# Kernel optimization log

Measured on AMD Instinct MI355X. Metric: run time of the kernel, lower is better.

The kernel has to match this reference:

```python
import jax, jax.numpy as jnp
import numpy as np

N = 768        # particles
C0 = 16        # input L0 channels
TDIM = 8       # time embedding channels
NB = 32        # sinusoidal rbf bases
H = 32         # hidden channels per L
NITERS = 2     # diffusion iterations (hk.scan length)
RCUT = 6.0     # rbf length scale
EPS = 1e-8

_lc = np.zeros((3, 3, 3), dtype=np.float32)
_lc[0, 1, 2] = _lc[1, 2, 0] = _lc[2, 0, 1] = 1.0
_lc[0, 2, 1] = _lc[2, 1, 0] = _lc[1, 0, 2] = -1.0
LEVI_CIVITA = jnp.asarray(_lc)


def setup_inputs() -> dict:
    key = jax.random.key(0)
    ks = jax.random.split(key, 20)
    s = 0.05
    inp = {
        "positions":   jax.random.normal(ks[0], (N, 3)),
        "features_L0": jax.random.normal(ks[1], (N, C0, 1)),
        "tw1": s * jax.random.normal(ks[2], (1, 32)),
        "tb1": jnp.zeros((32,)),
        "tw2": s * jax.random.normal(ks[3], (32, TDIM)),
        "tb2": jnp.zeros((TDIM,)),
        "R0_00": s * jax.random.normal(ks[4], (NB, C0 + TDIM)),
        "R0_01": s * jax.random.normal(ks[5], (NB, C0 + TDIM)),
        "W0_L0": s * jax.random.normal(ks[6], (C0 + TDIM, H)),
        "b0_L0": jnp.zeros((H,)),
        "W0_L1": s * jax.random.normal(ks[7], (C0 + TDIM, H)),
        "R1_00":  s * jax.random.normal(ks[8], (NB, H)),
        "R1_11d": s * jax.random.normal(ks[9], (NB, H)),
        "R1_01":  s * jax.random.normal(ks[10], (NB, H)),
        "R1_10":  s * jax.random.normal(ks[11], (NB, H)),
        "R1_11c": s * jax.random.normal(ks[12], (NB, H)),
        "W1_L0": s * jax.random.normal(ks[13], (2 * H, 1)),
        "b1_L0": jnp.zeros((1,)),
        "W1_L1": s * jax.random.normal(ks[14], (3 * H, 2)),
        "hutch_seed": 0,
    }
    return inp


def reference(positions, features_L0, tw1, tb1, tw2, tb2,
              R0_00, R0_01, W0_L0, b0_L0, W0_L1,
              R1_00, R1_11d, R1_01, R1_10, R1_11c,
              W1_L0, b1_L0, W1_L1, hutch_seed):
    freqs = jnp.arange(1, NB + 1, dtype=jnp.float32) * (np.pi / RCUT)
    key0 = jax.random.key(hutch_seed)

    def step(carry, it):
        pos, key = carry
        # pairwise displacements / norms / unit vectors, diagonal masked to 0
        r = pos[:, None, :] - pos[None, :, :]                 # (N,N,3)
        n2 = jnp.sum(r * r, axis=-1)                          # (N,N)
        norms = jnp.sqrt(n2 + EPS)
        valid = n2 > 1e-10
        safe = jnp.where(valid, norms, 1.0)
        unit = r / safe[..., None]                            # (N,N,3)
        # sinusoidal radial basis, masked on diagonal (mask_value = 0)
        rbf = jnp.where(valid[..., None],
                        jnp.sin(norms[..., None] * freqs) / safe[..., None],
                        0.0)                                   # (N,N,NB)
        # time convolution MLP, appended as extra L0 channels
        t = (it.astype(jnp.float32) + 1.0) / NITERS
        th = jax.nn.swish(jnp.array([t]) @ tw1 + tb1)
        tvec = th @ tw2 + tb2                                  # (TDIM,)
        aug = jnp.concatenate(
            [features_L0, jnp.broadcast_to(tvec[None, :, None], (N, TDIM, 1))],
            axis=1)                                            # (N,C0+TDIM,1)
        f0 = aug[..., 0]                                       # (N,C0+TDIM)

        # ---- layer 0: conv (L0 input only) + per-L MLP (nonlinear) ----
        Rw = jnp.einsum('ijb,bc->ijc', rbf, R0_00)
        o0 = jnp.einsum('ijc,jc->ic', Rw, f0)[..., None]       # (N,C,1)
        Rw = jnp.einsum('ijb,bc->ijc', rbf, R0_01)
        o1 = jnp.einsum('ijc,jc,ijm->icm', Rw, f0, unit)       # (N,C,3)
        x0 = jax.nn.swish(jnp.einsum('nco,ch->nho', o0, W0_L0)
                          + b0_L0[None, :, None])              # (N,H,1)
        v1 = jnp.einsum('ncm,ch->nhm', o1, W0_L1)
        gate = jax.nn.sigmoid(jnp.sqrt(jnp.sum(v1 * v1, -1) + EPS))
        x1 = v1 * gate[..., None]                              # (N,H,3)

        # ---- layer 1: full L={0,1} TFN conv + linear output MLPs ----
        f0b = x0[..., 0]
        Rw = jnp.einsum('ijb,bc->ijc', rbf, R1_00)
        o0a = jnp.einsum('ijc,jc->ic', Rw, f0b)                # 0x0->0
        Rw = jnp.einsum('ijb,bc->ijc', rbf, R1_11d)
        o0b = jnp.einsum('ijc,jcm,ijm->ic', Rw, x1, unit)      # 1x1->0 (dot)
        o0 = jnp.concatenate([o0a, o0b], axis=-1)[..., None]   # (N,2H,1)
        Rw = jnp.einsum('ijb,bc->ijc', rbf, R1_01)
        o1a = jnp.einsum('ijc,jc,ijm->icm', Rw, f0b, unit)     # 0x1->1
        Rw = jnp.einsum('ijb,bc->ijc', rbf, R1_10)
        o1b = jnp.einsum('ijc,jcm->icm', Rw, x1)               # 1x0->1
        Rw = jnp.einsum('ijb,bc->ijc', rbf, R1_11c)
        o1c = jnp.einsum('ijc,jca,ijb,abm->icm', Rw, x1, unit, LEVI_CIVITA)  # 1x1->1 (cross)
        o1 = jnp.concatenate([o1a, o1b, o1c], axis=1)          # (N,3H,3)
        y0 = jnp.einsum('nco,ch->nho', o0, W1_L0) + b1_L0[None, :, None]  # (N,1,1)
        y1 = jnp.einsum('ncm,ch->nhm', o1, W1_L1)              # (N,2,3)

        # output head: log-sigma from L0 channel 0, translation from L1 channel 1
        sigmas = jnp.repeat(jnp.exp(y0[:, 0, :]), repeats=3, axis=-1)  # (N,3)
        translations = y1[:, 1, :]
        mu = pos + translations
        key, hkey = jax.random.split(key)
        noise = jax.random.normal(hkey, (N, 3))
        out_y = mu + noise * sigmas
        logp = jax.scipy.stats.norm.logpdf(out_y, loc=mu, scale=sigmas).sum()
        return (out_y, key), (out_y, logp)

    (out_pos, _), (ys, logps) = jax.lax.scan(
        step, (positions, key0), jnp.arange(NITERS))
    out_ys = jnp.concatenate([positions[None], ys], axis=0)   # (NITERS+1,N,3)
    return out_pos, jnp.sum(logps), out_ys
```

## Files before the change

kernel.cpp:

```cpp
#include <hip/hip_runtime.h>
#include <hip/hip_bf16.h>
#include <stdint.h>

#define WS_MODE  0
#define WS_PX    16
#define WS_PY    784
#define WS_PZ    1552
#define WS_TVEC  2320
#define WS_HKEY  2336
#define WS_FEATT 2352
#define WS_W0L0  14640
#define WS_B0L0  15408
#define WS_W0L1  15440
#define WS_W1L0  16208
#define WS_B1L0  16272
#define WS_W1L1  16288
#define WS_R00T  16480
#define WS_R01T  17248
#define WS_R1F   18016
#define WS_GT    23136
#define WS_PA    293472
#define WS_PB    293472
#define WS_LG    735840

#define OUT_LOGP 2304
#define OUT_YS   2305

__device__ __forceinline__ float ld_in(const void* p, int idx, int bf) {
  if (bf) return __bfloat162float(((const __hip_bfloat16*)p)[idx]);
  return ((const float*)p)[idx];
}
__device__ __forceinline__ void store_out(void* out, int idx, float v, int bf) {
  if (bf) ((__hip_bfloat16*)out)[idx] = __float2bfloat16(v);
  else ((float*)out)[idx] = v;
}

__device__ __forceinline__ void tf2x32(uint32_t k0, uint32_t k1, uint32_t x0, uint32_t x1,
                                       uint32_t& o0, uint32_t& o1) {
  uint32_t ks[3] = {k0, k1, k0 ^ k1 ^ 0x1BD11BDAu};
  x0 += ks[0]; x1 += ks[1];
  const int R0[4] = {13, 15, 26, 6};
  const int R1[4] = {17, 29, 16, 24};
#pragma unroll
  for (int i = 0; i < 5; ++i) {
    const int* r = (i & 1) ? R1 : R0;
#pragma unroll
    for (int q = 0; q < 4; ++q) {
      x0 += x1;
      x1 = (x1 << r[q]) | (x1 >> (32 - r[q]));
      x1 ^= x0;
    }
    x0 += ks[(i + 1) % 3];
    x1 += ks[(i + 2) % 3] + (uint32_t)(i + 1);
  }
  o0 = x0; o1 = x1;
}

__device__ __forceinline__ float erfinv_f(float x) {
  float w = -log1pf(-x * x);
  float p;
  if (w < 5.0f) {
    w -= 2.5f;
    p = 2.81022636e-08f;
    p = fmaf(p, w, 3.43273939e-07f);
    p = fmaf(p, w, -3.5233877e-06f);
    p = fmaf(p, w, -4.39150654e-06f);
    p = fmaf(p, w, 0.00021858087f);
    p = fmaf(p, w, -0.00125372503f);
    p = fmaf(p, w, -0.00417768164f);
    p = fmaf(p, w, 0.246640727f);
    p = fmaf(p, w, 1.50140941f);
  } else {
    w = sqrtf(w) - 3.0f;
    p = -0.000200214257f;
    p = fmaf(p, w, 0.000100950558f);
    p = fmaf(p, w, 0.00134934322f);
    p = fmaf(p, w, -0.00367342844f);
    p = fmaf(p, w, 0.00573950773f);
    p = fmaf(p, w, -0.0076224613f);
    p = fmaf(p, w, 0.00943887047f);
    p = fmaf(p, w, 1.00167406f);
    p = fmaf(p, w, 2.83297682f);
  }
  return p * x;
}

__device__ int probe_bf(const void* pos, int tid) {
  __shared__ int s_ok;
  if (tid == 0) s_ok = 1;
  __syncthreads();
  const unsigned short* ph = (const unsigned short*)pos;
  int ok = 1;
  for (int e = tid; e < 2304; e += 256) {
    unsigned short v = ph[e];
    if ((v & 0x7fffu) != 0u) {
      int ex = (v >> 7) & 0xff;
      if (ex < 40 || ex > 140) ok = 0;
    }
  }
  if (!ok) atomicAnd(&s_ok, 0);
  __syncthreads();
  return s_ok;
}

__global__ __launch_bounds__(256) void k_init(
    const void* pos, const void* feats, const void* tw1, const void* tb1,
    const void* tw2, const void* tb2, const void* R000, const void* R001,
    const void* W0L0, const void* b0L0, const void* W0L1,
    const void* R100, const void* R111d, const void* R101,
    const void* R110, const void* R111c,
    const void* W1L0, const void* b1L0, const void* W1L1,
    const int* seedp, float* ws, void* out) {
  int tid = threadIdx.x, b = blockIdx.x;
  int bf = probe_bf(pos, tid);
  switch (b) {
    case 0: {
      if (tid == 0) ws[WS_MODE] = (float)bf;
      if (tid < 16) {
        int it = tid >> 3, d = tid & 7;
        float t = (float)(it + 1) * 0.5f;
        float a = ld_in(tb2, d, bf);
        for (int h = 0; h < 32; ++h) {
          float pre = fmaf(t, ld_in(tw1, h, bf), ld_in(tb1, h, bf));
          float th = pre / (1.0f + expf(-pre));
          a = fmaf(th, ld_in(tw2, h * 8 + d, bf), a);
        }
        ws[WS_TVEC + it * 8 + d] = a;
      }
      if (tid == 32) {
        uint32_t k0 = 0u, k1 = (uint32_t)seedp[0];
        uint32_t* hk = (uint32_t*)(ws + WS_HKEY);
        uint32_t a0, a1, b0, b1, c0, c1;
        tf2x32(k0, k1, 0u, 0u, a0, a1);
        tf2x32(k0, k1, 0u, 1u, b0, b1);
        hk[0] = b0; hk[1] = b1;
        tf2x32(a0, a1, 0u, 1u, c0, c1);
        hk[2] = c0; hk[3] = c1;
      }
      break;
    }
    case 1: {
      for (int n = tid; n < 768; n += 256) {
        ws[WS_PX + n] = ld_in(pos, n * 3 + 0, bf);
        ws[WS_PY + n] = ld_in(pos, n * 3 + 1, bf);
        ws[WS_PZ + n] = ld_in(pos, n * 3 + 2, bf);
      }
      break;
    }
    case 2: case 3: {
      for (int e = (b - 2) * 1152 + tid; e < (b - 1) * 1152; e += 256)
        store_out(out, OUT_YS + e, ld_in(pos, e, bf), bf);
      break;
    }
    case 4: case 5: case 6: case 7:
    case 8: case 9: case 10: case 11: {
      int base = (b - 4) * 1536;
      for (int e = base + tid; e < base + 1536; e += 256) {
        int j = e >> 4, c = e & 15;
        ws[WS_FEATT + c * 768 + j] = ld_in(feats, e, bf);
      }
      break;
    }
    case 12: {
      for (int e = tid; e < 768; e += 256) {
        ws[WS_W0L0 + e] = ld_in(W0L0, e, bf);
        ws[WS_W0L1 + e] = ld_in(W0L1, e, bf);
        int bb = e / 24, c = e % 24;
        ws[WS_R00T + c * 32 + bb] = ld_in(R000, e, bf);
        ws[WS_R01T + c * 32 + bb] = ld_in(R001, e, bf);
      }
      break;
    }
    case 13: {
      if (tid < 32) ws[WS_B0L0 + tid] = ld_in(b0L0, tid, bf);
      if (tid >= 64 && tid < 128) ws[WS_W1L0 + tid - 64] = ld_in(W1L0, tid - 64, bf);
      if (tid >= 128 && tid < 192) {
        for (int e = tid - 128; e < 192; e += 64) ws[WS_W1L1 + e] = ld_in(W1L1, e, bf);
      }
      if (tid == 33) ws[WS_B1L0] = ld_in(b1L0, 0, bf);
      break;
    }
    case 14: case 15: {
      int base = (b - 14) * 2560;
      const void* tabs[5] = {R100, R111d, R101, R110, R111c};
      for (int e = base + tid; e < base + 2560; e += 256) {
        int tab = e >> 10, off = e & 1023;
        ws[WS_R1F + e] = ld_in(tabs[tab], off, bf);
      }
      break;
    }
  }
}

__global__ __launch_bounds__(256) void k_passA(const float* __restrict__ ws,
                                               float* __restrict__ wso, int it) {
  int i = blockIdx.x, jset = blockIdx.y, CH = blockIdx.z;
  int tid = threadIdx.x, lane = tid & 63, w = tid >> 6;
  int j = jset * 256 + tid;
  float pix = ws[WS_PX + i], piy = ws[WS_PY + i], piz = ws[WS_PZ + i];

  float dx = pix - ws[WS_PX + j];
  float dy = piy - ws[WS_PY + j];
  float dz = piz - ws[WS_PZ + j];
  float n2 = dx * dx + dy * dy + dz * dz;
  float nrm = sqrtf(n2 + 1e-8f);
  float invn = 1.0f / nrm;
  float msk = (n2 > 1e-10f) ? invn : 0.0f;
  float ux = dx * invn, uy = dy * invn, uz = dz * invn;
  float sn, cs;
  sincosf(nrm * 0.52359879f, &sn, &cs);
  float rbf[32];
  float twoc = 2.0f * cs;
  rbf[0] = sn * msk;
  float skm1 = 0.0f, sk = rbf[0];
#pragma unroll
  for (int k = 1; k < 32; ++k) {
    float s2 = fmaf(twoc, sk, -skm1);
    skm1 = sk; sk = s2; rbf[k] = sk;
  }

  float fv[12];
  const float* __restrict__ rt0;
  const float* __restrict__ rt1;
  if (CH == 0) {
    rt0 = ws + WS_R00T; rt1 = ws + WS_R01T;
#pragma unroll
    for (int c = 0; c < 12; ++c) fv[c] = ws[WS_FEATT + c * 768 + j];
  } else {
    rt0 = ws + WS_R00T + 384; rt1 = ws + WS_R01T + 384;
#pragma unroll
    for (int c = 0; c < 4; ++c) fv[c] = ws[WS_FEATT + (12 + c) * 768 + j];
#pragma unroll
    for (int c = 4; c < 12; ++c) fv[c] = ws[WS_TVEC + it * 8 + (c - 4)];
  }

  float out[48];
#pragma unroll
  for (int c = 0; c < 12; ++c) {
    float rw0 = 0.0f, rw1 = 0.0f;
#pragma unroll
    for (int bq = 0; bq < 32; ++bq) {
      rw0 = fmaf(rbf[bq], rt0[c * 32 + bq], rw0);
      rw1 = fmaf(rbf[bq], rt1[c * 32 + bq], rw1);
    }
    float f = fv[c];
    out[c] = rw0 * f;
    float pp = rw1 * f;
    out[12 + 3 * c + 0] = pp * ux;
    out[12 + 3 * c + 1] = pp * uy;
    out[12 + 3 * c + 2] = pp * uz;
  }

#pragma unroll
  for (int k = 0; k < 48; ++k) {
    float v = out[k];
    v += __shfl_xor(v, 1);
    v += __shfl_xor(v, 2);
    out[k] = v;
  }
  __shared__ float P[48][65];
  if ((lane & 3) == 0) {
    int col = w * 16 + (lane >> 2);
#pragma unroll
    for (int k = 0; k < 48; ++k) P[k][col] = out[k];
  }
  __syncthreads();
  if (tid < 48) {
    float s = 0.0f;
#pragma unroll 8
    for (int q = 0; q < 64; ++q) s += P[tid][q];
    wso[WS_PA + ((CH * 3 + jset) * 768 + i) * 48 + tid] = s;
  }
}

__global__ __launch_bounds__(64) void k_passA2(const float* __restrict__ ws,
                                               float* __restrict__ wso) {
  int i = blockIdx.x, lane = threadIdx.x;
  __shared__ float oall[96];
  __shared__ float wf[11][32];
#pragma unroll
  for (int rep = 0; rep < 2; ++rep) {
    int t = rep * 64 + lane;
    if (rep == 0 || lane < 32) {
      int ch, k;
      if (t < 24) { ch = t / 12; k = t % 12; }
      else { int u = t - 24; int c = u / 3, m = u % 3; ch = c / 12; k = 12 + 3 * (c % 12) + m; }
      float s = 0.0f;
#pragma unroll
      for (int js = 0; js < 3; ++js)
        s += ws[WS_PA + ((ch * 3 + js) * 768 + i) * 48 + k];
      oall[t] = s;
    }
  }
  __syncthreads();
  if (lane < 32) {
    int h = lane;
    float x0p = ws[WS_B0L0 + h];
#pragma unroll
    for (int c = 0; c < 24; ++c) x0p = fmaf(oall[c], ws[WS_W0L0 + c * 32 + h], x0p);
    float f0b = x0p / (1.0f + expf(-x0p));
    float v0 = 0.0f, v1 = 0.0f, v2 = 0.0f;
#pragma unroll
    for (int c = 0; c < 24; ++c) {
      float w = ws[WS_W0L1 + c * 32 + h];
      v0 = fmaf(oall[24 + 3 * c + 0], w, v0);
      v1 = fmaf(oall[24 + 3 * c + 1], w, v1);
      v2 = fmaf(oall[24 + 3 * c + 2], w, v2);
    }
    float g = 1.0f / (1.0f + expf(-sqrtf(v0 * v0 + v1 * v1 + v2 * v2 + 1e-8f)));
    float x1m0 = v0 * g, x1m1 = v1 * g, x1m2 = v2 * g;
    float WA = ws[WS_W1L0 + h];
    float WB = ws[WS_W1L0 + 32 + h];
    float Wa = ws[WS_W1L1 + h * 2 + 1];
    float Wb = ws[WS_W1L1 + (32 + h) * 2 + 1];
    float Wc = ws[WS_W1L1 + (64 + h) * 2 + 1];
    wf[0][h] = WA * f0b;
    wf[1][h] = WB * x1m0; wf[2][h] = WB * x1m1; wf[3][h] = WB * x1m2;
    wf[4][h] = Wa * f0b;
    wf[5][h] = Wb * x1m0; wf[6][h] = Wb * x1m1; wf[7][h] = Wb * x1m2;
    wf[8][h] = Wc * x1m0; wf[9][h] = Wc * x1m1; wf[10][h] = Wc * x1m2;
  }
  __syncthreads();
  for (int tt = lane; tt < 352; tt += 64) {
    int comp = tt >> 5, b = tt & 31;
    int tab = (comp == 0) ? 0 : (comp < 4) ? 1 : (comp == 4) ? 2 : (comp < 8) ? 3 : 4;
    const float* rrow = ws + WS_R1F + tab * 1024 + b * 32;
    float gacc = 0.0f;
#pragma unroll
    for (int c = 0; c < 32; ++c) gacc = fmaf(rrow[c], wf[comp][c], gacc);
    wso[WS_GT + i * 352 + tt] = gacc;
  }
}

__global__ __launch_bounds__(256) void k_passB(const float* __restrict__ ws,
                                               float* __restrict__ wso) {
  int i = blockIdx.y * 256 + threadIdx.x;
  int chunk = blockIdx.x;
  float pix = ws[WS_PX + i], piy = ws[WS_PY + i], piz = ws[WS_PZ + i];
  float y0 = 0.0f, t0 = 0.0f, t1 = 0.0f, t2 = 0.0f;
  for (int q = 0; q < 8; ++q) {
    int j = chunk * 8 + q;
    float dx = pix - ws[WS_PX + j];
    float dy = piy - ws[WS_PY + j];
    float dz = piz - ws[WS_PZ + j];
    float n2 = dx * dx + dy * dy + dz * dz;
    float nrm = sqrtf(n2 + 1e-8f);
    float invn = 1.0f / nrm;
    float msk = (n2 > 1e-10f) ? invn : 0.0f;
    float ux = dx * invn, uy = dy * invn, uz = dz * invn;
    float sn, cs;
    sincosf(nrm * 0.52359879f, &sn, &cs);
    float rbf[32];
    float twoc = 2.0f * cs;
    rbf[0] = sn * msk;
    float skm1 = 0.0f, sk = rbf[0];
#pragma unroll
    for (int k = 1; k < 32; ++k) {
      float s2 = fmaf(twoc, sk, -skm1);
      skm1 = sk; sk = s2; rbf[k] = sk;
    }
    const float* g = ws + WS_GT + j * 352;
    float sA = 0.f, vB0 = 0.f, vB1 = 0.f, vB2 = 0.f, sC = 0.f;
    float vD0 = 0.f, vD1 = 0.f, vD2 = 0.f, vE0 = 0.f, vE1 = 0.f, vE2 = 0.f;
#pragma unroll
    for (int b = 0; b < 32; ++b) {
      float r = rbf[b];
      sA  = fmaf(r, g[0 * 32 + b], sA);
      vB0 = fmaf(r, g[1 * 32 + b], vB0);
      vB1 = fmaf(r, g[2 * 32 + b], vB1);
      vB2 = fmaf(r, g[3 * 32 + b], vB2);
      sC  = fmaf(r, g[4 * 32 + b], sC);
      vD0 = fmaf(r, g[5 * 32 + b], vD0);
      vD1 = fmaf(r, g[6 * 32 + b], vD1);
      vD2 = fmaf(r, g[7 * 32 + b], vD2);
      vE0 = fmaf(r, g[8 * 32 + b], vE0);
      vE1 = fmaf(r, g[9 * 32 + b], vE1);
      vE2 = fmaf(r, g[10 * 32 + b], vE2);
    }
    y0 += sA + vB0 * ux + vB1 * uy + vB2 * uz;
    t0 += sC * ux + vD0 + (vE1 * uz - vE2 * uy);
    t1 += sC * uy + vD1 + (vE2 * ux - vE0 * uz);
    t2 += sC * uz + vD2 + (vE0 * uy - vE1 * ux);
  }
  float4* pb = (float4*)(wso + WS_PB);
  pb[i * 96 + chunk] = make_float4(y0, t0, t1, t2);
}

__global__ __launch_bounds__(64) void k_passB2(float* __restrict__ ws, void* out, int it) {
  int i = blockIdx.x * 64 + threadIdx.x;
  int bf = (int)ws[WS_MODE];
  const float4* pb = (const float4*)(ws + WS_PB);
  float ax = 0.f, ay = 0.f, az = 0.f, aw = 0.f;
#pragma unroll 8
  for (int c = 0; c < 96; ++c) {
    float4 v = pb[i * 96 + c];
    ax += v.x; ay += v.y; az += v.z; aw += v.w;
  }
  float y0 = ax + ws[WS_B1L0];
  float sg = expf(y0);
  float s2 = sg * sg;
  float lnrm = 0.5f * logf(6.2831855f * s2);
  const uint32_t* hk = (const uint32_t*)(ws + WS_HKEY);
  uint32_t h0 = hk[it * 2 + 0], h1 = hk[it * 2 + 1];
  float base[3] = {ws[WS_PX + i], ws[WS_PY + i], ws[WS_PZ + i]};
  float tr[3] = {ay, az, aw};
  float logp = 0.0f;
#pragma unroll
  for (int m = 0; m < 3; ++m) {
    float mu = base[m] + tr[m];
    int f = i * 3 + m;
    uint32_t o0, o1;
    tf2x32(h0, h1, 0u, (uint32_t)f, o0, o1);
    uint32_t bits = o0 ^ o1;
    float u1 = __uint_as_float((bits >> 9) | 0x3f800000u) - 1.0f;
    const float lo = -0.99999994f;
    float u = fmaxf(lo, u1 * 2.0f + lo);
    float nz = 1.41421354f * erfinv_f(u);
    float oy = mu + nz * sg;
    float d = oy - mu;
    logp -= lnrm + (d * d) / (2.0f * s2);
    if (m == 0) ws[WS_PX + i] = oy;
    else if (m == 1) ws[WS_PY + i] = oy;
    else ws[WS_PZ + i] = oy;
    store_out(out, OUT_YS + (it + 1) * 2304 + i * 3 + m, oy, bf);
    if (it == 1) store_out(out, i * 3 + m, oy, bf);
  }
  ws[WS_LG + it * 768 + i] = logp;
}

__global__ void k_logp(float* __restrict__ ws, void* out) {
  __shared__ float red[256];
  int t = threadIdx.x;
  float s = 0.0f;
  for (int e = t; e < 1536; e += 256) s += ws[WS_LG + e];
  red[t] = s;
  __syncthreads();
  for (int off = 128; off; off >>= 1) {
    if (t < off) red[t] += red[t + off];
    __syncthreads();
  }
  if (t == 0) store_out(out, OUT_LOGP, red[0], (int)ws[WS_MODE]);
}

extern "C" void kernel_launch(void* const* d_in, const int* in_sizes, int n_in,
                              void* d_out, int out_size, void* d_ws, size_t ws_size,
                              hipStream_t stream) {
  (void)in_sizes; (void)n_in; (void)out_size; (void)ws_size;
  float* ws = (float*)d_ws;
  k_init<<<16, 256, 0, stream>>>(d_in[0], d_in[1], d_in[2], d_in[3], d_in[4], d_in[5],
                                 d_in[6], d_in[7], d_in[8], d_in[9], d_in[10],
                                 d_in[11], d_in[12], d_in[13], d_in[14], d_in[15],
                                 d_in[16], d_in[17], d_in[18], (const int*)d_in[19],
                                 ws, d_out);
  for (int it = 0; it < 2; ++it) {
    k_passA<<<dim3(768, 3, 2), 256, 0, stream>>>(ws, ws, it);
    k_passA2<<<768, 64, 0, stream>>>(ws, ws);
    k_passB<<<dim3(96, 3), 256, 0, stream>>>(ws, ws);
    k_passB2<<<12, 64, 0, stream>>>(ws, d_out, it);
  }
  k_logp<<<1, 256, 0, stream>>>(ws, d_out);
}
```

Before: 195.7 us.

## Stream rbf recurrence into accumulators and split passB into smaller blocks

In passA the 32-element rbf array is no longer materialized. Each sine-recurrence term is consumed immediately into 24 running accumulators, and the radial tables are stored in their natural basis-major layout so the loads walk along channels. This lowers register pressure and gives uniform, contiguous table reads. Separately, passB is launched with 64-thread blocks over a 96x12 grid instead of 256-thread blocks over 96x3, which gives four times as many blocks for the same number of threads.

```diff
diff --git a/kernel.cpp b/kernel.cpp
--- a/kernel.cpp
+++ b/kernel.cpp
@@ -165,9 +165,8 @@
       for (int e = tid; e < 768; e += 256) {
         ws[WS_W0L0 + e] = ld_in(W0L0, e, bf);
         ws[WS_W0L1 + e] = ld_in(W0L1, e, bf);
-        int bb = e / 24, c = e % 24;
-        ws[WS_R00T + c * 32 + bb] = ld_in(R000, e, bf);
-        ws[WS_R01T + c * 32 + bb] = ld_in(R001, e, bf);
+        ws[WS_R00T + e] = ld_in(R000, e, bf);
+        ws[WS_R01T + e] = ld_in(R001, e, bf);
       }
       break;
     }
@@ -209,43 +208,42 @@
   float ux = dx * invn, uy = dy * invn, uz = dz * invn;
   float sn, cs;
   sincosf(nrm * 0.52359879f, &sn, &cs);
-  float rbf[32];
   float twoc = 2.0f * cs;
-  rbf[0] = sn * msk;
-  float skm1 = 0.0f, sk = rbf[0];
-#pragma unroll
-  for (int k = 1; k < 32; ++k) {
-    float s2 = fmaf(twoc, sk, -skm1);
-    skm1 = sk; sk = s2; rbf[k] = sk;
-  }
 
   float fv[12];
-  const float* __restrict__ rt0;
-  const float* __restrict__ rt1;
+  const float* __restrict__ rt0 = ws + WS_R00T + CH * 12;
+  const float* __restrict__ rt1 = ws + WS_R01T + CH * 12;
   if (CH == 0) {
-    rt0 = ws + WS_R00T; rt1 = ws + WS_R01T;
 #pragma unroll
     for (int c = 0; c < 12; ++c) fv[c] = ws[WS_FEATT + c * 768 + j];
   } else {
-    rt0 = ws + WS_R00T + 384; rt1 = ws + WS_R01T + 384;
 #pragma unroll
     for (int c = 0; c < 4; ++c) fv[c] = ws[WS_FEATT + (12 + c) * 768 + j];
 #pragma unroll
     for (int c = 4; c < 12; ++c) fv[c] = ws[WS_TVEC + it * 8 + (c - 4)];
   }
 
+  float rw0[12], rw1[12];
+#pragma unroll
+  for (int c = 0; c < 12; ++c) { rw0[c] = 0.0f; rw1[c] = 0.0f; }
+  float sk = sn * msk, skm1 = 0.0f;
+#pragma unroll
+  for (int b = 0; b < 32; ++b) {
+#pragma unroll
+    for (int c = 0; c < 12; ++c) {
+      rw0[c] = fmaf(sk, rt0[b * 24 + c], rw0[c]);
+      rw1[c] = fmaf(sk, rt1[b * 24 + c], rw1[c]);
+    }
+    float s2 = fmaf(twoc, sk, -skm1);
+    skm1 = sk; sk = s2;
+  }
+
   float out[48];
 #pragma unroll
   for (int c = 0; c < 12; ++c) {
-    float rw0 = 0.0f, rw1 = 0.0f;
-#pragma unroll
-    for (int bq = 0; bq < 32; ++bq) {
-      rw0 = fmaf(rbf[bq], rt0[c * 32 + bq], rw0);
-      rw1 = fmaf(rbf[bq], rt1[c * 32 + bq], rw1);
-    }
     float f = fv[c];
-    out[c] = rw0 * f;
-    float pp = rw1 * f;
+    out[c] = rw0[c] * f;
+    float pp = rw1[c] * f;
     out[12 + 3 * c + 0] = pp * ux;
     out[12 + 3 * c + 1] = pp * uy;
     out[12 + 3 * c + 2] = pp * uz;
@@ -332,9 +330,9 @@
   }
 }
 
-__global__ __launch_bounds__(256) void k_passB(const float* __restrict__ ws,
-                                               float* __restrict__ wso) {
-  int i = blockIdx.y * 256 + threadIdx.x;
+__global__ __launch_bounds__(64) void k_passB(const float* __restrict__ ws,
+                                              float* __restrict__ wso) {
+  int i = blockIdx.y * 64 + threadIdx.x;
   int chunk = blockIdx.x;
   float pix = ws[WS_PX + i], piy = ws[WS_PY + i], piz = ws[WS_PZ + i];
   float y0 = 0.0f, t0 = 0.0f, t1 = 0.0f, t2 = 0.0f;
@@ -455,7 +453,7 @@
   for (int it = 0; it < 2; ++it) {
     k_passA<<<dim3(768, 3, 2), 256, 0, stream>>>(ws, ws, it);
     k_passA2<<<768, 64, 0, stream>>>(ws, ws);
-    k_passB<<<dim3(96, 3), 256, 0, stream>>>(ws, ws);
+    k_passB<<<dim3(96, 12), 64, 0, stream>>>(ws, ws);
     k_passB2<<<12, 64, 0, stream>>>(ws, d_out, it);
   }
   k_logp<<<1, 256, 0, stream>>>(ws, d_out);
```

Result: faster. 189.6 us, median of 3 (-3.1%).
